# Kernel optimization log

Measured on AMD Instinct MI355X. Metric: run time of the kernel, lower is better.

Reference implementation:

```python
import jax, jax.numpy as jnp
import numpy as np

T = 16            # hardcoded timesteps in DQSN.forward
V_TH = 1.0        # IFNode default v_threshold
TAU = 2.0         # NonSpikingLIFNode tau
SG_ALPHA = 4.0    # spikingjelly surrogate.Sigmoid alpha


@jax.custom_vjp
def spike_fn(x):
    # Heaviside step with sigmoid surrogate gradient (spikingjelly default).
    return (x >= 0.0).astype(x.dtype)

def _spike_fwd(x):
    return spike_fn(x), x

def _spike_bwd(x, g):
    s = jax.nn.sigmoid(SG_ALPHA * x)
    return (g * SG_ALPHA * s * (1.0 - s),)

spike_fn.defvjp(_spike_fwd, _spike_bwd)


def setup_inputs() -> dict:
    key = jax.random.key(0)
    ks = jax.random.split(key, 5)
    B, H = 16384, 4096
    x = jax.random.normal(ks[0], (B, 4), dtype=jnp.float32)
    W1 = jax.random.normal(ks[1], (H, 4), dtype=jnp.float32) * 0.5   # Linear(4, H)
    b1 = jax.random.normal(ks[2], (H,), dtype=jnp.float32) * 0.1
    W2 = jax.random.normal(ks[3], (2, H), dtype=jnp.float32) * 0.02  # Linear(H, 2)
    b2 = jax.random.normal(ks[4], (2,), dtype=jnp.float32) * 0.1
    return {"x": x, "W1": W1, "b1": b1, "W2": W2, "b2": b2}


def reference(x, W1, b1, W2, b2):
    B = x.shape[0]
    H = W1.shape[0]
    # Input current is constant across the T steps (same x every step).
    I1 = x @ W1.T + b1                        # [B, H]

    def step(carry, _):
        v1, v2 = carry
        # IFNode: charge, spike (hard reset to v_reset=0)
        v1 = v1 + I1
        s = spike_fn(v1 - V_TH)               # [B, H]
        v1 = v1 * (1.0 - s)
        # Linear(H, 2) -> NonSpikingLIFNode: v += (dv - (v - 0)) / tau
        dv = s @ W2.T + b2                    # [B, 2]
        v2 = v2 + (dv - v2) / TAU
        return (v1, v2), None

    v1_0 = jnp.zeros((B, H), dtype=x.dtype)
    v2_0 = jnp.zeros((B, 2), dtype=x.dtype)
    (v1, v2), _ = jax.lax.scan(step, (v1_0, v2_0), None, length=T)
    return v2
```

## Files before the change

### kernel.cpp

```cpp
#include <hip/hip_runtime.h>


constexpr int TSTEPS = 16;
constexpr int NB = 8;
constexpr float GUARD = 4e-5f;

template <int CITERS>
__global__ __launch_bounds__(256) void dqsn_fwd(
    const float* __restrict__ x,
    const float* __restrict__ W1,
    const float* __restrict__ b1,
    const float* __restrict__ W2,
    const float* __restrict__ b2,
    float* __restrict__ out,
    int B, int H, int iters_rt)
{
    const int tid  = threadIdx.x;
    const int lane = tid & 63;
    const int b0   = blockIdx.x * NB;

    float tval = 0.0f;
    if (lane >= 1 && lane <= TSTEPS) {
        unsigned mm = 0;
        for (int k = lane; k <= TSTEPS; k += lane) mm |= 1u << (k - 1);
        tval = (float)mm * 0x1p-16f;
    }
    const int table_reg = __float_as_int(tval);

    float xs0[NB], xs1[NB], xs2[NB], xs3[NB];
#pragma unroll
    for (int i = 0; i < NB; ++i) {
        const int bi = (b0 + i < B) ? (b0 + i) : (B - 1);
        xs0[i] = x[bi * 4 + 0];
        xs1[i] = x[bi * 4 + 1];
        xs2[i] = x[bi * 4 + 2];
        xs3[i] = x[bi * 4 + 3];
    }

    float acc0[NB], acc1[NB];
#pragma unroll
    for (int i = 0; i < NB; ++i) { acc0[i] = 0.0f; acc1[i] = 0.0f; }

    const int iters = (CITERS > 0) ? CITERS : iters_rt;

#pragma unroll 4
    for (int it = 0; it < iters; ++it) {
        const int h = tid + (it << 8);
        const float4 w1 = *reinterpret_cast<const float4*>(W1 + (size_t)h * 4);
        const float bb  = b1[h];
        const float w2a = W2[h];
        const float w2b = W2[H + h];

        float I[NB];
        int   idx[NB];
        float e[NB];
#pragma unroll
        for (int i = 0; i < NB; ++i) {
            I[i] = fmaf(xs0[i], w1.x,
                   fmaf(xs1[i], w1.y,
                   fmaf(xs2[i], w1.z,
                   fmaf(xs3[i], w1.w, bb))));
            const float r = __builtin_amdgcn_rcpf(I[i]);
            const float c = __builtin_ceilf(r);
            const float m = __builtin_amdgcn_fmed3f(c, 0.0f, 17.0f);
            idx[i] = (int)m << 2;
            e[i] = (r - c) + 0.5f;
        }

        float g0 = fmaxf(fmaxf(fabsf(e[0]), fabsf(e[1])), fabsf(e[2]));
        float g1 = fmaxf(fmaxf(fabsf(e[3]), fabsf(e[4])), fabsf(e[5]));
        float g2 = fmaxf(fabsf(e[6]), fabsf(e[7]));
        const float gmax = fmaxf(fmaxf(g0, g1), g2);

        if (__builtin_expect((unsigned long long)__ballot(gmax > 0.5f - GUARD), 0)) {
#pragma unroll
            for (int i = 0; i < NB; ++i) {
                float v = 0.0f;
                int cnt = 0;
#pragma unroll
                for (int t = 0; t < TSTEPS; ++t) {
                    v += I[i];
                    cnt += (v < 1.0f) ? 1 : 0;
                }
                idx[i] = (cnt + 1 <= 16 ? cnt + 1 : 17) << 2;
            }
        }

#pragma unroll
        for (int i = 0; i < NB; ++i) {
            const float A = __int_as_float(__builtin_amdgcn_ds_bpermute(idx[i], table_reg));
            acc0[i] = fmaf(A, w2a, acc0[i]);
            acc1[i] = fmaf(A, w2b, acc1[i]);
        }
    }

#pragma unroll
    for (int i = 0; i < NB; ++i) {
#pragma unroll
        for (int off = 32; off > 0; off >>= 1) {
            acc0[i] += __shfl_xor(acc0[i], off, 64);
            acc1[i] += __shfl_xor(acc1[i], off, 64);
        }
    }

    __shared__ float red[4][NB][2];
    const int wave = tid >> 6;
    if ((tid & 63) == 0) {
#pragma unroll
        for (int i = 0; i < NB; ++i) {
            red[wave][i][0] = acc0[i];
            red[wave][i][1] = acc1[i];
        }
    }
    __syncthreads();

    if (tid < NB * 2) {
        const int i = tid >> 1;
        const int o = tid & 1;
        if (b0 + i < B) {
            const float s = ((red[0][i][o] + red[1][i][o]) +
                             (red[2][i][o] + red[3][i][o]))
                          + b2[o] * (1.0f - 0x1p-16f);
            out[(b0 + i) * 2 + o] = s;
        }
    }
}

extern "C" void kernel_launch(void* const* d_in, const int* in_sizes, int n_in,
                              void* d_out, int out_size, void* d_ws, size_t ws_size,
                              hipStream_t stream) {
    const float* x  = (const float*)d_in[0];
    const float* W1 = (const float*)d_in[1];
    const float* b1 = (const float*)d_in[2];
    const float* W2 = (const float*)d_in[3];
    const float* b2 = (const float*)d_in[4];
    float* out = (float*)d_out;

    const int B = in_sizes[0] / 4;
    const int H = in_sizes[2];

    const int grid = (B + NB - 1) / NB;
    if (H == 4096) {
        dqsn_fwd<16><<<grid, 256, 0, stream>>>(x, W1, b1, W2, b2, out, B, H, 16);
    } else {
        dqsn_fwd<0><<<grid, 256, 0, stream>>>(x, W1, b1, W2, b2, out, B, H, H / 256);
    }
}
```

Measured before the change: 39.77 us.

## Halve rows per block, software-prefetch weights, and apply slow-path correction as delta

Each block now handles 4 batch rows instead of 8, which doubles the grid. The unrolled loop is replaced by a non-unrolled loop that loads the next iteration's W1/b1/W2 values while computing on the current ones. The table lookup and accumulation now run unconditionally. The rare exact-simulation fallback adds a correction (new minus old table value) instead of recomputing the index first. This is meant to hide global-load latency and cut register pressure, but it doubles the redundant weight reads per batch row and loses unrolling.

After: 39.15 us. Within noise of the previous version (-1.5%).

```diff
diff --git a/kernel.cpp b/kernel.cpp
--- a/kernel.cpp
+++ b/kernel.cpp
@@ -2,7 +2,7 @@
 
 
 constexpr int TSTEPS = 16;
-constexpr int NB = 8;
+constexpr int NB = 4;
 constexpr float GUARD = 4e-5f;
 
 template <int CITERS>
@@ -43,36 +43,43 @@
 
     const int iters = (CITERS > 0) ? CITERS : iters_rt;
 
-#pragma unroll 4
+    float4 w1c = *reinterpret_cast<const float4*>(W1 + (size_t)tid * 4);
+    float  bbc = b1[tid];
+    float  w2ac = W2[tid];
+    float  w2bc = W2[H + tid];
+
+#pragma unroll 1
     for (int it = 0; it < iters; ++it) {
-        const int h = tid + (it << 8);
-        const float4 w1 = *reinterpret_cast<const float4*>(W1 + (size_t)h * 4);
-        const float bb  = b1[h];
-        const float w2a = W2[h];
-        const float w2b = W2[H + h];
+        const int hn = (it + 1 < iters) ? (tid + (it + 1) * 256) : tid;
+        const float4 w1n = *reinterpret_cast<const float4*>(W1 + (size_t)hn * 4);
+        const float  bbn = b1[hn];
+        const float  w2an = W2[hn];
+        const float  w2bn = W2[H + hn];
 
         float I[NB];
         int   idx[NB];
-        float e[NB];
+        float emax = 0.0f;
 #pragma unroll
         for (int i = 0; i < NB; ++i) {
-            I[i] = fmaf(xs0[i], w1.x,
-                   fmaf(xs1[i], w1.y,
-                   fmaf(xs2[i], w1.z,
-                   fmaf(xs3[i], w1.w, bb))));
+            I[i] = fmaf(xs0[i], w1c.x,
+                   fmaf(xs1[i], w1c.y,
+                   fmaf(xs2[i], w1c.z,
+                   fmaf(xs3[i], w1c.w, bbc))));
             const float r = __builtin_amdgcn_rcpf(I[i]);
             const float c = __builtin_ceilf(r);
             const float m = __builtin_amdgcn_fmed3f(c, 0.0f, 17.0f);
             idx[i] = (int)m << 2;
-            e[i] = (r - c) + 0.5f;
+            emax = fmaxf(emax, fabsf((r - c) + 0.5f));
         }
 
-        float g0 = fmaxf(fmaxf(fabsf(e[0]), fabsf(e[1])), fabsf(e[2]));
-        float g1 = fmaxf(fmaxf(fabsf(e[3]), fabsf(e[4])), fabsf(e[5]));
-        float g2 = fmaxf(fabsf(e[6]), fabsf(e[7]));
-        const float gmax = fmaxf(fmaxf(g0, g1), g2);
+#pragma unroll
+        for (int i = 0; i < NB; ++i) {
+            const float A = __int_as_float(__builtin_amdgcn_ds_bpermute(idx[i], table_reg));
+            acc0[i] = fmaf(A, w2ac, acc0[i]);
+            acc1[i] = fmaf(A, w2bc, acc1[i]);
+        }
 
-        if (__builtin_expect((unsigned long long)__ballot(gmax > 0.5f - GUARD), 0)) {
+        if (__builtin_expect((unsigned long long)__ballot(emax > 0.5f - GUARD), 0)) {
 #pragma unroll
             for (int i = 0; i < NB; ++i) {
                 float v = 0.0f;
@@ -82,16 +89,16 @@
                     v += I[i];
                     cnt += (v < 1.0f) ? 1 : 0;
                 }
-                idx[i] = (cnt + 1 <= 16 ? cnt + 1 : 17) << 2;
+                const int idx2 = (cnt + 1) << 2;
+                const float An = __int_as_float(__builtin_amdgcn_ds_bpermute(idx2, table_reg));
+                const float Ao = __int_as_float(__builtin_amdgcn_ds_bpermute(idx[i], table_reg));
+                const float dA = An - Ao;
+                acc0[i] = fmaf(dA, w2ac, acc0[i]);
+                acc1[i] = fmaf(dA, w2bc, acc1[i]);
             }
         }
 
-#pragma unroll
-        for (int i = 0; i < NB; ++i) {
-            const float A = __int_as_float(__builtin_amdgcn_ds_bpermute(idx[i], table_reg));
-            acc0[i] = fmaf(A, w2a, acc0[i]);
-            acc1[i] = fmaf(A, w2b, acc1[i]);
-        }
+        w1c = w1n; bbc = bbn; w2ac = w2an; w2bc = w2bn;
     }
 
 #pragma unroll
```

## Software-pipeline weight loads and spike-count lookup across hidden-unit iterations

Applied to the files above, without the earlier changes.

Restructures the main loop into a software pipeline. Weights are prefetched two iterations ahead, and the current-and-reciprocal computation plus the bpermute table lookup for the next iteration runs in the same loop body. The rare fallback path now applies a correction delta to the accumulators instead of recomputing the index before the lookup. The aim is to hide global-load and LDS-permute latency, at the cost of more registers and a peeled epilogue.

Measured after the change: 38.95 us. -2.0%, faster.

```diff
diff --git a/kernel.cpp b/kernel.cpp
--- a/kernel.cpp
+++ b/kernel.cpp
@@ -4,6 +4,7 @@
 constexpr int TSTEPS = 16;
 constexpr int NB = 8;
 constexpr float GUARD = 4e-5f;
+constexpr float GTHR  = 0.5f - GUARD;
 
 template <int CITERS>
 __global__ __launch_bounds__(256) void dqsn_fwd(
@@ -43,54 +44,111 @@
 
     const int iters = (CITERS > 0) ? CITERS : iters_rt;
 
+    float4 w1B; float bbB, w2aB, w2bB;
+    {
+        const int h1 = (1 < iters) ? tid + 256 : tid;
+        w1B  = *reinterpret_cast<const float4*>(W1 + (size_t)h1 * 4);
+        bbB  = b1[h1];
+        w2aB = W2[h1];
+        w2bB = W2[H + h1];
+    }
+
+    float I_c[NB]; int idx_c[NB]; float A_c[NB];
+    float em_c;
+    float w2a_c, w2b_c;
+    {
+        const float4 w1 = *reinterpret_cast<const float4*>(W1 + (size_t)tid * 4);
+        const float  bb = b1[tid];
+        w2a_c = W2[tid];
+        w2b_c = W2[H + tid];
+        em_c = 0.0f;
+#pragma unroll
+        for (int i = 0; i < NB; ++i) {
+            I_c[i] = fmaf(xs0[i], w1.x,
+                     fmaf(xs1[i], w1.y,
+                     fmaf(xs2[i], w1.z,
+                     fmaf(xs3[i], w1.w, bb))));
+            const float r = __builtin_amdgcn_rcpf(I_c[i]);
+            const float c = __builtin_ceilf(r);
+            idx_c[i] = (int)__builtin_amdgcn_fmed3f(c, 0.0f, 17.0f) << 2;
+            em_c = fmaxf(em_c, fabsf((r - c) + 0.5f));
+        }
+#pragma unroll
+        for (int i = 0; i < NB; ++i)
+            A_c[i] = __int_as_float(__builtin_amdgcn_ds_bpermute(idx_c[i], table_reg));
+    }
+
 #pragma unroll 4
-    for (int it = 0; it < iters; ++it) {
-        const int h = tid + (it << 8);
-        const float4 w1 = *reinterpret_cast<const float4*>(W1 + (size_t)h * 4);
-        const float bb  = b1[h];
-        const float w2a = W2[h];
-        const float w2b = W2[H + h];
-
-        float I[NB];
-        int   idx[NB];
-        float e[NB];
-#pragma unroll
-        for (int i = 0; i < NB; ++i) {
-            I[i] = fmaf(xs0[i], w1.x,
-                   fmaf(xs1[i], w1.y,
-                   fmaf(xs2[i], w1.z,
-                   fmaf(xs3[i], w1.w, bb))));
-            const float r = __builtin_amdgcn_rcpf(I[i]);
-            const float c = __builtin_ceilf(r);
-            const float m = __builtin_amdgcn_fmed3f(c, 0.0f, 17.0f);
-            idx[i] = (int)m << 2;
-            e[i] = (r - c) + 0.5f;
-        }
-
-        float g0 = fmaxf(fmaxf(fabsf(e[0]), fabsf(e[1])), fabsf(e[2]));
-        float g1 = fmaxf(fmaxf(fabsf(e[3]), fabsf(e[4])), fabsf(e[5]));
-        float g2 = fmaxf(fabsf(e[6]), fabsf(e[7]));
-        const float gmax = fmaxf(fmaxf(g0, g1), g2);
-
-        if (__builtin_expect((unsigned long long)__ballot(gmax > 0.5f - GUARD), 0)) {
+    for (int it = 0; it < iters - 1; ++it) {
+        const int h2 = (it + 2 < iters) ? tid + (it + 2) * 256 : tid;
+        const float4 w1N  = *reinterpret_cast<const float4*>(W1 + (size_t)h2 * 4);
+        const float  bbN  = b1[h2];
+        const float  w2aN = W2[h2];
+        const float  w2bN = W2[H + h2];
+
+#pragma unroll
+        for (int i = 0; i < NB; ++i) {
+            acc0[i] = fmaf(A_c[i], w2a_c, acc0[i]);
+            acc1[i] = fmaf(A_c[i], w2b_c, acc1[i]);
+        }
+        if (__builtin_expect((unsigned long long)__ballot(em_c > GTHR), 0)) {
 #pragma unroll
             for (int i = 0; i < NB; ++i) {
                 float v = 0.0f;
                 int cnt = 0;
 #pragma unroll
                 for (int t = 0; t < TSTEPS; ++t) {
-                    v += I[i];
+                    v += I_c[i];
                     cnt += (v < 1.0f) ? 1 : 0;
                 }
-                idx[i] = (cnt + 1 <= 16 ? cnt + 1 : 17) << 2;
+                const float An = __int_as_float(
+                    __builtin_amdgcn_ds_bpermute((cnt + 1) << 2, table_reg));
+                const float dA = An - A_c[i];
+                acc0[i] = fmaf(dA, w2a_c, acc0[i]);
+                acc1[i] = fmaf(dA, w2b_c, acc1[i]);
             }
         }
 
-#pragma unroll
-        for (int i = 0; i < NB; ++i) {
-            const float A = __int_as_float(__builtin_amdgcn_ds_bpermute(idx[i], table_reg));
-            acc0[i] = fmaf(A, w2a, acc0[i]);
-            acc1[i] = fmaf(A, w2b, acc1[i]);
+        em_c = 0.0f;
+#pragma unroll
+        for (int i = 0; i < NB; ++i) {
+            I_c[i] = fmaf(xs0[i], w1B.x,
+                     fmaf(xs1[i], w1B.y,
+                     fmaf(xs2[i], w1B.z,
+                     fmaf(xs3[i], w1B.w, bbB))));
+            const float r = __builtin_amdgcn_rcpf(I_c[i]);
+            const float c = __builtin_ceilf(r);
+            idx_c[i] = (int)__builtin_amdgcn_fmed3f(c, 0.0f, 17.0f) << 2;
+            em_c = fmaxf(em_c, fabsf((r - c) + 0.5f));
+        }
+#pragma unroll
+        for (int i = 0; i < NB; ++i)
+            A_c[i] = __int_as_float(__builtin_amdgcn_ds_bpermute(idx_c[i], table_reg));
+        w2a_c = w2aB; w2b_c = w2bB;
+
+        w1B = w1N; bbB = bbN; w2aB = w2aN; w2bB = w2bN;
+    }
+
+#pragma unroll
+    for (int i = 0; i < NB; ++i) {
+        acc0[i] = fmaf(A_c[i], w2a_c, acc0[i]);
+        acc1[i] = fmaf(A_c[i], w2b_c, acc1[i]);
+    }
+    if (__builtin_expect((unsigned long long)__ballot(em_c > GTHR), 0)) {
+#pragma unroll
+        for (int i = 0; i < NB; ++i) {
+            float v = 0.0f;
+            int cnt = 0;
+#pragma unroll
+            for (int t = 0; t < TSTEPS; ++t) {
+                v += I_c[i];
+                cnt += (v < 1.0f) ? 1 : 0;
+            }
+            const float An = __int_as_float(
+                __builtin_amdgcn_ds_bpermute((cnt + 1) << 2, table_reg));
+            const float dA = An - A_c[i];
+            acc0[i] = fmaf(dA, w2a_c, acc0[i]);
+            acc1[i] = fmaf(dA, w2b_c, acc1[i]);
         }
     }
 
```

## Compute spike count closed-form via bitreverse and reduce through LDS transpose

Applied to the files above, without the earlier changes.

Replaces the per-lane ds_bpermute table lookup with arithmetic: the scaled spike-pattern value is built from 2^n-1 reciprocal and a 32-bit bit-reverse. The fallback path now applies a delta correction to the accumulators instead of rewriting indices. The cross-lane shuffle reduction is replaced by an LDS transpose-and-sum in two stages, with a final 2^-32 rescale. This removes the LDS-permute traffic in the hot loop and the many shuffles at the end, at the cost of more ALU work per element, a 20KB shared buffer, and reliance on exact rounding of the rcp-based formula.

Measured after the change: 53.68 us. +35.0%, slower.

```diff
diff --git a/kernel.cpp b/kernel.cpp
--- a/kernel.cpp
+++ b/kernel.cpp
@@ -4,6 +4,17 @@
 constexpr int TSTEPS = 16;
 constexpr int NB = 8;
 constexpr float GUARD = 4e-5f;
+constexpr float GTHR  = 0.5f - GUARD;
+
+__device__ __forceinline__ float A_scaled(float nf) {
+    const int   ni = (int)nf;
+    const float p  = __builtin_amdgcn_ldexpf(1.0f, ni);
+    const float q  = p - 1.0f;
+    const float t  = __builtin_amdgcn_rcpf(q);
+    const float u  = fmaf(t, 65535.0f, 0.5f);
+    const unsigned qu = (unsigned)u;
+    return (float)__builtin_bitreverse32(qu);
+}
 
 template <int CITERS>
 __global__ __launch_bounds__(256) void dqsn_fwd(
@@ -15,17 +26,8 @@
     float* __restrict__ out,
     int B, int H, int iters_rt)
 {
-    const int tid  = threadIdx.x;
-    const int lane = tid & 63;
-    const int b0   = blockIdx.x * NB;
-
-    float tval = 0.0f;
-    if (lane >= 1 && lane <= TSTEPS) {
-        unsigned mm = 0;
-        for (int k = lane; k <= TSTEPS; k += lane) mm |= 1u << (k - 1);
-        tval = (float)mm * 0x1p-16f;
-    }
-    const int table_reg = __float_as_int(tval);
+    const int tid = threadIdx.x;
+    const int b0  = blockIdx.x * NB;
 
     float xs0[NB], xs1[NB], xs2[NB], xs3[NB];
 #pragma unroll
@@ -51,9 +53,8 @@
         const float w2a = W2[h];
         const float w2b = W2[H + h];
 
-        float I[NB];
-        int   idx[NB];
-        float e[NB];
+        float I[NB], As[NB];
+        float emax = 0.0f;
 #pragma unroll
         for (int i = 0; i < NB; ++i) {
             I[i] = fmaf(xs0[i], w1.x,
@@ -62,17 +63,19 @@
                    fmaf(xs3[i], w1.w, bb))));
             const float r = __builtin_amdgcn_rcpf(I[i]);
             const float c = __builtin_ceilf(r);
-            const float m = __builtin_amdgcn_fmed3f(c, 0.0f, 17.0f);
-            idx[i] = (int)m << 2;
-            e[i] = (r - c) + 0.5f;
+            const float nf = __builtin_amdgcn_fmed3f(c, 1.0f, 17.0f);
+            float A = A_scaled(nf);
+            As[i] = (c > 0.0f) ? A : 0.0f;
+            emax = fmaxf(emax, fabsf((r - c) + 0.5f));
         }
 
-        float g0 = fmaxf(fmaxf(fabsf(e[0]), fabsf(e[1])), fabsf(e[2]));
-        float g1 = fmaxf(fmaxf(fabsf(e[3]), fabsf(e[4])), fabsf(e[5]));
-        float g2 = fmaxf(fabsf(e[6]), fabsf(e[7]));
-        const float gmax = fmaxf(fmaxf(g0, g1), g2);
+#pragma unroll
+        for (int i = 0; i < NB; ++i) {
+            acc0[i] = fmaf(As[i], w2a, acc0[i]);
+            acc1[i] = fmaf(As[i], w2b, acc1[i]);
+        }
 
-        if (__builtin_expect((unsigned long long)__ballot(gmax > 0.5f - GUARD), 0)) {
+        if (__builtin_expect((unsigned long long)__ballot(emax > GTHR), 0)) {
 #pragma unroll
             for (int i = 0; i < NB; ++i) {
                 float v = 0.0f;
@@ -82,47 +85,47 @@
                     v += I[i];
                     cnt += (v < 1.0f) ? 1 : 0;
                 }
-                idx[i] = (cnt + 1 <= 16 ? cnt + 1 : 17) << 2;
+                const float An = A_scaled((float)(cnt + 1));
+                const float dA = An - As[i];
+                acc0[i] = fmaf(dA, w2a, acc0[i]);
+                acc1[i] = fmaf(dA, w2b, acc1[i]);
             }
-        }
-
-#pragma unroll
-        for (int i = 0; i < NB; ++i) {
-            const float A = __int_as_float(__builtin_amdgcn_ds_bpermute(idx[i], table_reg));
-            acc0[i] = fmaf(A, w2a, acc0[i]);
-            acc1[i] = fmaf(A, w2b, acc1[i]);
         }
     }
 
-#pragma unroll
-    for (int i = 0; i < NB; ++i) {
-#pragma unroll
-        for (int off = 32; off > 0; off >>= 1) {
-            acc0[i] += __shfl_xor(acc0[i], off, 64);
-            acc1[i] += __shfl_xor(acc1[i], off, 64);
-        }
-    }
+    __shared__ float lds[256 * 20];
+    __shared__ float lds2[256];
 
-    __shared__ float red[4][NB][2];
-    const int wave = tid >> 6;
-    if ((tid & 63) == 0) {
-#pragma unroll
-        for (int i = 0; i < NB; ++i) {
-            red[wave][i][0] = acc0[i];
-            red[wave][i][1] = acc1[i];
-        }
+    {
+        float* base = &lds[tid * 20];
+        *reinterpret_cast<float4*>(base +  0) = (float4){acc0[0], acc1[0], acc0[1], acc1[1]};
+        *reinterpret_cast<float4*>(base +  4) = (float4){acc0[2], acc1[2], acc0[3], acc1[3]};
+        *reinterpret_cast<float4*>(base +  8) = (float4){acc0[4], acc1[4], acc0[5], acc1[5]};
+        *reinterpret_cast<float4*>(base + 12) = (float4){acc0[6], acc1[6], acc0[7], acc1[7]};
     }
     __syncthreads();
 
-    if (tid < NB * 2) {
-        const int i = tid >> 1;
-        const int o = tid & 1;
-        if (b0 + i < B) {
-            const float s = ((red[0][i][o] + red[1][i][o]) +
-                             (red[2][i][o] + red[3][i][o]))
-                          + b2[o] * (1.0f - 0x1p-16f);
-            out[(b0 + i) * 2 + o] = s;
-        }
+    {
+        const int o = tid & 15;
+        const int j = tid >> 4;
+        float s = 0.0f;
+#pragma unroll
+        for (int k = 0; k < 16; ++k)
+            s += lds[(j + 16 * k) * 20 + o];
+        lds2[tid] = s;
+    }
+    __syncthreads();
+
+    if (tid < 16) {
+        float tot = 0.0f;
+#pragma unroll
+        for (int j = 0; j < 16; ++j)
+            tot += lds2[j * 16 + tid];
+        const int i  = tid >> 1;
+        const int oo = tid & 1;
+        if (b0 + i < B)
+            out[(b0 + i) * 2 + oo] =
+                fmaf(tot, 0x1p-32f, b2[oo] * (1.0f - 0x1p-16f));
     }
 }
 
```
